# Optimization experiments

Measured on AMD Instinct MI355X. Metric: run time of the kernel, lower is better.

## Reference

```python
import jax, jax.numpy as jnp
import numpy as np

IN = 1    # input feature dim (hardcoded in NN)
H = 10    # LSTM hidden size (hardcoded in NN)
B = 8192  # batch
T = 256   # sequence length


def setup_inputs() -> dict:
    key = jax.random.key(0)
    ks = jax.random.split(key, 12)
    s = 0.1  # init scale for mus (mimics blitz posterior_mu_init spread)
    RHO0 = -3.0  # posterior_rho_init from the module
    return {
        "x": jax.random.normal(ks[0], (B, T, IN), jnp.float32),
        # BayesianLSTM variational parameters (blitz layout: (in, 4*H), (H, 4*H), (4*H,))
        "w_ih_mu": jax.random.normal(ks[1], (IN, 4 * H), jnp.float32) * s,
        "w_ih_rho": jnp.full((IN, 4 * H), RHO0, jnp.float32),
        "w_hh_mu": jax.random.normal(ks[2], (H, 4 * H), jnp.float32) * s,
        "w_hh_rho": jnp.full((H, 4 * H), RHO0, jnp.float32),
        "b_mu": jax.random.normal(ks[3], (4 * H,), jnp.float32) * s,
        "b_rho": jnp.full((4 * H,), RHO0, jnp.float32),
        # reparameterization noise, sampled once per forward call in blitz
        "eps_ih": jax.random.normal(ks[4], (IN, 4 * H), jnp.float32),
        "eps_hh": jax.random.normal(ks[5], (H, 4 * H), jnp.float32),
        "eps_b": jax.random.normal(ks[6], (4 * H,), jnp.float32),
        # deterministic linear head nn.Linear(10, 1)
        "lin_w": jax.random.normal(ks[7], (1, H), jnp.float32) * s,
        "lin_b": jnp.zeros((1,), jnp.float32),
    }


def reference(x, w_ih_mu, w_ih_rho, w_hh_mu, w_hh_rho, b_mu, b_rho,
              eps_ih, eps_hh, eps_b, lin_w, lin_b):
    sp = jax.nn.softplus
    # sample weights: w = mu + log1p(exp(rho)) * eps
    w_ih = w_ih_mu + sp(w_ih_rho) * eps_ih   # (IN, 4H)
    w_hh = w_hh_mu + sp(w_hh_rho) * eps_hh   # (H, 4H)
    b = b_mu + sp(b_rho) * eps_b             # (4H,)

    # precompute input contribution for all timesteps: (B, T, 4H)
    x_proj = jnp.einsum('bti,ig->btg', x, w_ih) + b

    def step(carry, xg):
        h, c = carry                      # (B, H) each
        gates = xg + h @ w_hh             # (B, 4H)
        i = jax.nn.sigmoid(gates[:, :H])
        f = jax.nn.sigmoid(gates[:, H:2 * H])
        g = jnp.tanh(gates[:, 2 * H:3 * H])
        o = jax.nn.sigmoid(gates[:, 3 * H:])
        c = f * c + i * g
        h = o * jnp.tanh(c)
        return (h, c), None

    h0 = jnp.zeros((x.shape[0], H), x.dtype)
    (h_last, _), _ = jax.lax.scan(step, (h0, h0), jnp.swapaxes(x_proj, 0, 1))
    # NN takes hidden_seq[:, -1, :] == final hidden state, then linear head
    return h_last @ lin_w.T + lin_b  # (B, 1)
```

## Files before the change

### kernel.cpp

```cpp
#include <hip/hip_runtime.h>
#include <math.h>

#define T_LEN 256
#define HID 10

typedef float v2f __attribute__((ext_vector_type(2)));

__device__ __forceinline__ v2f mk2(float a, float b) { v2f r; r.x = a; r.y = b; return r; }
__device__ __forceinline__ v2f splat2(float a) { return mk2(a, a); }

__device__ __forceinline__ float softplus_f(float x) {
    return fmaxf(x, 0.0f) + log1pf(expf(-fabsf(x)));
}
__device__ __forceinline__ float samp(const float* mu, const float* rho,
                                      const float* eps, int i) {
    return mu[i] + softplus_f(rho[i]) * eps[i];
}

__device__ __forceinline__ float fast_sigmoid(float x) {
    float e = __builtin_amdgcn_exp2f(-1.442695040888963f * x);
    return __builtin_amdgcn_rcpf(1.0f + e);
}
__device__ __forceinline__ float fast_tanh(float x) {
    float e = __builtin_amdgcn_exp2f(2.885390081777927f * x);
    return fmaf(-2.0f, __builtin_amdgcn_rcpf(e + 1.0f), 1.0f);
}

struct Wreg {
    v2f whh01[HID], whh23[HID];
    v2f wih01, wih23, b01, b23;
};

__device__ __forceinline__ float lstm_step(const Wreg& w, float xt,
                                           float4 h0, float4 h1, float4 h2,
                                           float& c)
{
    v2f x2 = splat2(xt);
    v2f e01 = __builtin_elementwise_fma(x2, w.wih01, w.b01);
    v2f e23 = __builtin_elementwise_fma(x2, w.wih23, w.b23);
    v2f o01 = w.whh01[1] * splat2(h0.y);
    v2f o23 = w.whh23[1] * splat2(h0.y);
    e01 = __builtin_elementwise_fma(splat2(h0.x), w.whh01[0], e01);
    e23 = __builtin_elementwise_fma(splat2(h0.x), w.whh23[0], e23);
    o01 = __builtin_elementwise_fma(splat2(h0.w), w.whh01[3], o01);
    o23 = __builtin_elementwise_fma(splat2(h0.w), w.whh23[3], o23);
    e01 = __builtin_elementwise_fma(splat2(h0.z), w.whh01[2], e01);
    e23 = __builtin_elementwise_fma(splat2(h0.z), w.whh23[2], e23);
    o01 = __builtin_elementwise_fma(splat2(h1.y), w.whh01[5], o01);
    o23 = __builtin_elementwise_fma(splat2(h1.y), w.whh23[5], o23);
    e01 = __builtin_elementwise_fma(splat2(h1.x), w.whh01[4], e01);
    e23 = __builtin_elementwise_fma(splat2(h1.x), w.whh23[4], e23);
    o01 = __builtin_elementwise_fma(splat2(h1.w), w.whh01[7], o01);
    o23 = __builtin_elementwise_fma(splat2(h1.w), w.whh23[7], o23);
    e01 = __builtin_elementwise_fma(splat2(h1.z), w.whh01[6], e01);
    e23 = __builtin_elementwise_fma(splat2(h1.z), w.whh23[6], e23);
    o01 = __builtin_elementwise_fma(splat2(h2.y), w.whh01[9], o01);
    o23 = __builtin_elementwise_fma(splat2(h2.y), w.whh23[9], o23);
    e01 = __builtin_elementwise_fma(splat2(h2.x), w.whh01[8], e01);
    e23 = __builtin_elementwise_fma(splat2(h2.x), w.whh23[8], e23);
    v2f a01 = e01 + o01;
    v2f a23 = e23 + o23;
    float ig = fast_sigmoid(a01.x);
    float fg = fast_sigmoid(a01.y);
    float gg = fast_tanh(a23.x);
    float og = fast_sigmoid(a23.y);
    c = fmaf(fg, c, ig * gg);
    return og * fast_tanh(c);
}

__global__ __launch_bounds__(256) void bayes_lstm_kernel(
    const float* __restrict__ x,
    const float* __restrict__ w_ih_mu, const float* __restrict__ w_ih_rho,
    const float* __restrict__ w_hh_mu, const float* __restrict__ w_hh_rho,
    const float* __restrict__ b_mu,    const float* __restrict__ b_rho,
    const float* __restrict__ eps_ih,  const float* __restrict__ eps_hh,
    const float* __restrict__ eps_b,
    const float* __restrict__ lin_w,   const float* __restrict__ lin_b,
    float* __restrict__ out)
{
    __shared__ __align__(16) float hbuf[16 * 2 * 12];

    const int tid   = threadIdx.x;
    const int k     = tid & 15;
    const int slot  = tid >> 4;
    const int gslot = blockIdx.x * 16 + slot;
    const int bA    = gslot * 2, bB = bA + 1;
    const int ibA   = slot * 24, ibB = ibA + 12;

    Wreg w;
#pragma unroll
    for (int j = 0; j < HID; ++j) { w.whh01[j] = splat2(0.f); w.whh23[j] = splat2(0.f); }
    w.wih01 = splat2(0.f); w.wih23 = splat2(0.f);
    w.b01 = splat2(0.f);   w.b23 = splat2(0.f);
    float lw = 0.f;
    if (k < HID) {
        const int c0 = k, c1 = HID + k, c2 = 2 * HID + k, c3 = 3 * HID + k;
        w.wih01 = mk2(samp(w_ih_mu, w_ih_rho, eps_ih, c0), samp(w_ih_mu, w_ih_rho, eps_ih, c1));
        w.wih23 = mk2(samp(w_ih_mu, w_ih_rho, eps_ih, c2), samp(w_ih_mu, w_ih_rho, eps_ih, c3));
        w.b01   = mk2(samp(b_mu, b_rho, eps_b, c0), samp(b_mu, b_rho, eps_b, c1));
        w.b23   = mk2(samp(b_mu, b_rho, eps_b, c2), samp(b_mu, b_rho, eps_b, c3));
#pragma unroll
        for (int j = 0; j < HID; ++j) {
            w.whh01[j] = mk2(samp(w_hh_mu, w_hh_rho, eps_hh, j * 4 * HID + c0),
                             samp(w_hh_mu, w_hh_rho, eps_hh, j * 4 * HID + c1));
            w.whh23[j] = mk2(samp(w_hh_mu, w_hh_rho, eps_hh, j * 4 * HID + c2),
                             samp(w_hh_mu, w_hh_rho, eps_hh, j * 4 * HID + c3));
        }
        lw = lin_w[k];
        hbuf[ibA + k] = 0.f;
        hbuf[ibB + k] = 0.f;
    }

    float cA = 0.f, cB = 0.f, hkA = 0.f, hkB = 0.f;
    const float* xrA = x + (size_t)bA * T_LEN;
    const float* xrB = x + (size_t)bB * T_LEN;
    float xcA = xrA[k];
    float xcB = xrB[k];
    const float4* pA = (const float4*)(hbuf + ibA);
    const float4* pB = (const float4*)(hbuf + ibB);

    for (int to = 0; to < 16; ++to) {
        float xnA = 0.f, xnB = 0.f;
        if (to < 15) {
            xnA = xrA[(to + 1) * 16 + k];
            xnB = xrB[(to + 1) * 16 + k];
        }
#pragma unroll
        for (int ti = 0; ti < 16; ++ti) {
            float4 hA0 = pA[0], hA1 = pA[1], hA2 = pA[2];
            float4 hB0 = pB[0], hB1 = pB[1], hB2 = pB[2];
            float xa = __shfl(xcA, ti, 16);
            float xb = __shfl(xcB, ti, 16);
            hkA = lstm_step(w, xa, hA0, hA1, hA2, cA);
            hkB = lstm_step(w, xb, hB0, hB1, hB2, cB);
            if (k < HID) {
                hbuf[ibA + k] = hkA;
                hbuf[ibB + k] = hkB;
            }
        }
        xcA = xnA; xcB = xnB;
    }

    float pa = hkA * lw;
    float pb = hkB * lw;
    pa += __shfl_xor(pa, 1, 16);  pb += __shfl_xor(pb, 1, 16);
    pa += __shfl_xor(pa, 2, 16);  pb += __shfl_xor(pb, 2, 16);
    pa += __shfl_xor(pa, 4, 16);  pb += __shfl_xor(pb, 4, 16);
    pa += __shfl_xor(pa, 8, 16);  pb += __shfl_xor(pb, 8, 16);
    if (k == 0) {
        float b0 = lin_b[0];
        out[bA] = pa + b0;
        out[bB] = pb + b0;
    }
}

extern "C" void kernel_launch(void* const* d_in, const int* in_sizes, int n_in,
                              void* d_out, int out_size, void* d_ws, size_t ws_size,
                              hipStream_t stream) {
    const float* x        = (const float*)d_in[0];
    const float* w_ih_mu  = (const float*)d_in[1];
    const float* w_ih_rho = (const float*)d_in[2];
    const float* w_hh_mu  = (const float*)d_in[3];
    const float* w_hh_rho = (const float*)d_in[4];
    const float* b_mu     = (const float*)d_in[5];
    const float* b_rho    = (const float*)d_in[6];
    const float* eps_ih   = (const float*)d_in[7];
    const float* eps_hh   = (const float*)d_in[8];
    const float* eps_b    = (const float*)d_in[9];
    const float* lin_w    = (const float*)d_in[10];
    const float* lin_b    = (const float*)d_in[11];
    float* out = (float*)d_out;

    const int n_b = in_sizes[0] / T_LEN;
    dim3 grid(n_b / 32), block(256);
    hipLaunchKernelGGL(bayes_lstm_kernel, grid, block, 0, stream,
                       x, w_ih_mu, w_ih_rho, w_hh_mu, w_hh_rho, b_mu, b_rho,
                       eps_ih, eps_hh, eps_b, lin_w, lin_b, out);
}
```

Measured before the change: 164.3 us.

## Remap to ten lanes per batch row in 64-thread blocks

Restructures the thread mapping so each 64-lane wave runs six sequences with ten lanes each, one hidden unit per lane. This replaces sixteen-lane groups that each interleaved two sequences and left six lanes idle. The aim is to raise active lane use and cut the total number of waves' worth of step instructions. The final linear head now sums through shared memory instead of shuffles. The trade-off is losing the two-chain instruction-level parallelism inside each wave, and the waves now spread unevenly across SIMDs.

```diff
diff --git a/kernel.cpp b/kernel.cpp
--- a/kernel.cpp
+++ b/kernel.cpp
@@ -68,7 +68,7 @@
     return og * fast_tanh(c);
 }
 
-__global__ __launch_bounds__(256) void bayes_lstm_kernel(
+__global__ __launch_bounds__(64) void bayes_lstm_kernel(
     const float* __restrict__ x,
     const float* __restrict__ w_ih_mu, const float* __restrict__ w_ih_rho,
     const float* __restrict__ w_hh_mu, const float* __restrict__ w_hh_rho,
@@ -76,81 +76,62 @@
     const float* __restrict__ eps_ih,  const float* __restrict__ eps_hh,
     const float* __restrict__ eps_b,
     const float* __restrict__ lin_w,   const float* __restrict__ lin_b,
-    float* __restrict__ out)
+    float* __restrict__ out, int n_elem)
 {
-    __shared__ __align__(16) float hbuf[16 * 2 * 12];
+    __shared__ __align__(16) float hbuf[7 * 20];
 
-    const int tid   = threadIdx.x;
-    const int k     = tid & 15;
-    const int slot  = tid >> 4;
-    const int gslot = blockIdx.x * 16 + slot;
-    const int bA    = gslot * 2, bB = bA + 1;
-    const int ibA   = slot * 24, ibB = ibA + 12;
+    const int lane  = threadIdx.x;
+    const int g     = lane / 10;
+    const int k     = lane - g * 10;
+    const int gbase = g * 10;
+    const int b     = blockIdx.x * 6 + g;
+    const bool valid = (g < 6) && (b < n_elem);
+    const int b_eff = (b < n_elem) ? b : (n_elem - 1);
+    float* hb = hbuf + g * 20;
 
     Wreg w;
+    const int c0 = k, c1 = HID + k, c2 = 2 * HID + k, c3 = 3 * HID + k;
+    w.wih01 = mk2(samp(w_ih_mu, w_ih_rho, eps_ih, c0), samp(w_ih_mu, w_ih_rho, eps_ih, c1));
+    w.wih23 = mk2(samp(w_ih_mu, w_ih_rho, eps_ih, c2), samp(w_ih_mu, w_ih_rho, eps_ih, c3));
+    w.b01   = mk2(samp(b_mu, b_rho, eps_b, c0), samp(b_mu, b_rho, eps_b, c1));
+    w.b23   = mk2(samp(b_mu, b_rho, eps_b, c2), samp(b_mu, b_rho, eps_b, c3));
 #pragma unroll
-    for (int j = 0; j < HID; ++j) { w.whh01[j] = splat2(0.f); w.whh23[j] = splat2(0.f); }
-    w.wih01 = splat2(0.f); w.wih23 = splat2(0.f);
-    w.b01 = splat2(0.f);   w.b23 = splat2(0.f);
-    float lw = 0.f;
-    if (k < HID) {
-        const int c0 = k, c1 = HID + k, c2 = 2 * HID + k, c3 = 3 * HID + k;
-        w.wih01 = mk2(samp(w_ih_mu, w_ih_rho, eps_ih, c0), samp(w_ih_mu, w_ih_rho, eps_ih, c1));
-        w.wih23 = mk2(samp(w_ih_mu, w_ih_rho, eps_ih, c2), samp(w_ih_mu, w_ih_rho, eps_ih, c3));
-        w.b01   = mk2(samp(b_mu, b_rho, eps_b, c0), samp(b_mu, b_rho, eps_b, c1));
-        w.b23   = mk2(samp(b_mu, b_rho, eps_b, c2), samp(b_mu, b_rho, eps_b, c3));
+    for (int j = 0; j < HID; ++j) {
+        w.whh01[j] = mk2(samp(w_hh_mu, w_hh_rho, eps_hh, j * 4 * HID + c0),
+                         samp(w_hh_mu, w_hh_rho, eps_hh, j * 4 * HID + c1));
+        w.whh23[j] = mk2(samp(w_hh_mu, w_hh_rho, eps_hh, j * 4 * HID + c2),
+                         samp(w_hh_mu, w_hh_rho, eps_hh, j * 4 * HID + c3));
+    }
+    const float lw = lin_w[k];
+
+    hb[k] = 0.f;
+    if (k < 2) hb[10 + k] = 0.f;
+
+    float c = 0.f, hk = 0.f;
+    const float* xr = x + (size_t)b_eff * T_LEN;
+    const bool ldx = (k < 8);
+    float xc = ldx ? xr[k] : 0.f;
+    const float4* p = (const float4*)hb;
+
+    for (int ch = 0; ch < 32; ++ch) {
+        float xn = 0.f;
+        if (ldx && ch < 31) xn = xr[(ch + 1) * 8 + k];
 #pragma unroll
-        for (int j = 0; j < HID; ++j) {
-            w.whh01[j] = mk2(samp(w_hh_mu, w_hh_rho, eps_hh, j * 4 * HID + c0),
-                             samp(w_hh_mu, w_hh_rho, eps_hh, j * 4 * HID + c1));
-            w.whh23[j] = mk2(samp(w_hh_mu, w_hh_rho, eps_hh, j * 4 * HID + c2),
-                             samp(w_hh_mu, w_hh_rho, eps_hh, j * 4 * HID + c3));
+        for (int ti = 0; ti < 8; ++ti) {
+            float4 h0 = p[0], h1 = p[1], h2 = p[2];
+            float xt = __shfl(xc, gbase + ti, 64);
+            hk = lstm_step(w, xt, h0, h1, h2, c);
+            hb[k] = hk;
         }
-        lw = lin_w[k];
-        hbuf[ibA + k] = 0.f;
-        hbuf[ibB + k] = 0.f;
+        xc = xn;
     }
 
-    float cA = 0.f, cB = 0.f, hkA = 0.f, hkB = 0.f;
-    const float* xrA = x + (size_t)bA * T_LEN;
-    const float* xrB = x + (size_t)bB * T_LEN;
-    float xcA = xrA[k];
-    float xcB = xrB[k];
-    const float4* pA = (const float4*)(hbuf + ibA);
-    const float4* pB = (const float4*)(hbuf + ibB);
-
-    for (int to = 0; to < 16; ++to) {
-        float xnA = 0.f, xnB = 0.f;
-        if (to < 15) {
-            xnA = xrA[(to + 1) * 16 + k];
-            xnB = xrB[(to + 1) * 16 + k];
-        }
-#pragma unroll
-        for (int ti = 0; ti < 16; ++ti) {
-            float4 hA0 = pA[0], hA1 = pA[1], hA2 = pA[2];
-            float4 hB0 = pB[0], hB1 = pB[1], hB2 = pB[2];
-            float xa = __shfl(xcA, ti, 16);
-            float xb = __shfl(xcB, ti, 16);
-            hkA = lstm_step(w, xa, hA0, hA1, hA2, cA);
-            hkB = lstm_step(w, xb, hB0, hB1, hB2, cB);
-            if (k < HID) {
-                hbuf[ibA + k] = hkA;
-                hbuf[ibB + k] = hkB;
-            }
-        }
-        xcA = xnA; xcB = xnB;
-    }
-
-    float pa = hkA * lw;
-    float pb = hkB * lw;
-    pa += __shfl_xor(pa, 1, 16);  pb += __shfl_xor(pb, 1, 16);
-    pa += __shfl_xor(pa, 2, 16);  pb += __shfl_xor(pb, 2, 16);
-    pa += __shfl_xor(pa, 4, 16);  pb += __shfl_xor(pb, 4, 16);
-    pa += __shfl_xor(pa, 8, 16);  pb += __shfl_xor(pb, 8, 16);
-    if (k == 0) {
-        float b0 = lin_b[0];
-        out[bA] = pa + b0;
-        out[bB] = pb + b0;
+    hb[k] = hk * lw;
+    if (k == 0 && valid) {
+        float4 s0 = p[0], s1 = p[1], s2 = p[2];
+        out[b] = (s0.x + s0.y + s0.z + s0.w)
+               + (s1.x + s1.y + s1.z + s1.w)
+               + (s2.x + s2.y + s2.z + s2.w) + lin_b[0];
     }
 }
 
@@ -172,8 +153,8 @@
     float* out = (float*)d_out;
 
     const int n_b = in_sizes[0] / T_LEN;
-    dim3 grid(n_b / 32), block(256);
+    dim3 grid((n_b + 5) / 6), block(64);
     hipLaunchKernelGGL(bayes_lstm_kernel, grid, block, 0, stream,
                        x, w_ih_mu, w_ih_rho, w_hh_mu, w_hh_rho, b_mu, b_rho,
-                       eps_ih, eps_hh, eps_b, lin_w, lin_b, out);
+                       eps_ih, eps_hh, eps_b, lin_w, lin_b, out, n_b);
 }
```

Result: no change. 165.4 us (+0.7%).
